# Kernel optimization log

Measured on AMD Instinct MI355X. Metric: run time of the kernel, lower is better.

The kernel has to match this reference:

```python
import jax, jax.numpy as jnp
import numpy as np

D_MODEL = 256; D_FLOW = 128; D_FFN = 1024
N_HEADS = 8; N_LEVELS = 3; N_POINTS = 4
D_HEAD = D_MODEL // N_HEADS
SHAPES = np.array([[128, 128], [64, 64], [32, 32]], dtype=np.int64)


def setup_inputs():
    key = jax.random.key(0)
    ks = jax.random.split(key, 12)
    N = 2
    LeNin = int((SHAPES[:, 0] * SHAPES[:, 1]).sum())
    Lq = int(SHAPES[0, 0] * SHAPES[0, 1])
    lsi = np.concatenate([[0], np.cumsum(SHAPES[:, 0] * SHAPES[:, 1])[:-1]])
    s = 0.02
    return {
        'src': jax.random.normal(ks[0], (N, LeNin, D_MODEL), jnp.float32),
        'flow': jax.random.normal(ks[1], (N, Lq, D_FLOW), jnp.float32),
        'spatial_shapes': jnp.asarray(SHAPES, jnp.int32),
        'level_start_index': jnp.asarray(lsi, jnp.int32),
        'w_value': jax.random.normal(ks[2], (D_MODEL, D_MODEL), jnp.float32) * s,
        'b_value': jnp.zeros((D_MODEL,), jnp.float32),
        'w_off': jax.random.normal(ks[3], (D_FLOW, N_HEADS * N_LEVELS * N_POINTS * 2), jnp.float32) * s,
        'b_off': jax.random.normal(ks[4], (N_HEADS * N_LEVELS * N_POINTS * 2,), jnp.float32) * 0.5,
        'w_attn': jax.random.normal(ks[5], (D_FLOW, N_HEADS * N_LEVELS * N_POINTS), jnp.float32) * s,
        'b_attn': jnp.zeros((N_HEADS * N_LEVELS * N_POINTS,), jnp.float32),
        'w_out': jax.random.normal(ks[6], (D_MODEL, D_MODEL), jnp.float32) * s,
        'b_out': jnp.zeros((D_MODEL,), jnp.float32),
        'gamma': jnp.ones((D_MODEL,), jnp.float32),
        'beta': jnp.zeros((D_MODEL,), jnp.float32),
        'w1': jax.random.normal(ks[7], (D_MODEL, D_FFN), jnp.float32) * s,
        'b1': jnp.zeros((D_FFN,), jnp.float32),
        'w2': jax.random.normal(ks[8], (D_FFN, D_MODEL), jnp.float32) * s,
        'b2': jnp.zeros((D_MODEL,), jnp.float32),
    }


def _bilinear_level(v, xy, H, W):
    # v: [N, nh, H*W, dh]; xy: [N, Lq, nh, np, 2] normalized to [0,1]
    # grid_sample(align_corners=False) semantics: pixel = loc * size - 0.5, zero padding
    N, Lq = xy.shape[0], xy.shape[1]
    x = xy[..., 0] * W - 0.5
    y = xy[..., 1] * H - 0.5
    x0 = jnp.floor(x); y0 = jnp.floor(y)
    dx = x - x0; dy = y - y0
    acc = jnp.zeros((N, N_HEADS, Lq * N_POINTS, v.shape[-1]), v.dtype)
    corners = ((x0, y0, (1 - dx) * (1 - dy)),
               (x0 + 1, y0, dx * (1 - dy)),
               (x0, y0 + 1, (1 - dx) * dy),
               (x0 + 1, y0 + 1, dx * dy))
    for ix, iy, w in corners:
        valid = (ix >= 0) & (ix <= W - 1) & (iy >= 0) & (iy <= H - 1)
        xi = jnp.clip(ix, 0, W - 1).astype(jnp.int32)
        yi = jnp.clip(iy, 0, H - 1).astype(jnp.int32)
        idx = (yi * W + xi).transpose(0, 2, 1, 3).reshape(N, N_HEADS, Lq * N_POINTS)
        g = jnp.take_along_axis(v, idx[..., None], axis=2)  # [N, nh, Lq*np, dh]
        wv = (w * valid).transpose(0, 2, 1, 3).reshape(N, N_HEADS, Lq * N_POINTS, 1)
        acc = acc + wv * g
    return acc


def reference(src, flow, spatial_shapes, level_start_index, w_value, b_value,
              w_off, b_off, w_attn, b_attn, w_out, b_out, gamma, beta, w1, b1, w2, b2):
    ss = np.asarray(jax.device_get(spatial_shapes))
    lsi = np.asarray(jax.device_get(level_start_index))
    N, LeNin, _ = src.shape
    Lq = flow.shape[1]
    value = (src @ w_value + b_value).reshape(N, LeNin, N_HEADS, D_HEAD)
    off = (flow @ w_off + b_off).reshape(N, Lq, N_HEADS, N_LEVELS, N_POINTS, 2)
    attn = jax.nn.softmax((flow @ w_attn + b_attn).reshape(N, Lq, N_HEADS, N_LEVELS * N_POINTS), axis=-1)
    attn = attn.reshape(N, Lq, N_HEADS, N_LEVELS, N_POINTS)
    # reference points on level-0 grid (valid_ratios == 1)
    H0, W0 = int(ss[0, 0]), int(ss[0, 1])
    ry, rx = jnp.meshgrid(jnp.linspace(0.5, H0 - 0.5, H0) / H0,
                          jnp.linspace(0.5, W0 - 0.5, W0) / W0, indexing='ij')
    ref = jnp.stack([rx.reshape(-1), ry.reshape(-1)], -1)  # [Lq, 2] (x, y)
    norm = jnp.asarray(np.stack([ss[:, 1], ss[:, 0]], -1), jnp.float32)  # [nl, 2] = (W, H)
    loc = ref[None, :, None, None, None, :] + off / norm[None, None, None, :, None, :]
    acc = jnp.zeros((N, Lq, N_HEADS, D_HEAD), src.dtype)
    for l in range(N_LEVELS):
        H, W = int(ss[l, 0]), int(ss[l, 1])
        st = int(lsi[l])
        v = value[:, st:st + H * W].transpose(0, 2, 1, 3)  # [N, nh, HW, dh]
        s_l = _bilinear_level(v, loc[:, :, :, l], H, W).reshape(N, N_HEADS, Lq, N_POINTS, D_HEAD)
        acc = acc + jnp.einsum('bhqpd,bqhp->bqhd', s_l, attn[:, :, :, l])
    src2 = acc.reshape(N, Lq, D_MODEL) @ w_out + b_out
    x = src2  # dropout is identity at inference
    mu = x.mean(-1, keepdims=True)
    var = ((x - mu) ** 2).mean(-1, keepdims=True)
    ln = (x - mu) / jnp.sqrt(var + 1e-5) * gamma + beta
    ffn = jax.nn.relu(ln @ w1 + b1) @ w2 + b2
    return x + ffn
```

## Files before the change

kernel.cpp:

```cpp
#include <hip/hip_runtime.h>
#include <cstdint>
#include <cstddef>

#define D_MODEL  256
#define D_FLOW   128
#define D_FFN    1024
#define N_HEADS  8
#define N_LEVELS 3
#define N_POINTS 4
#define D_HEAD   32
#define LQ       16384
#define LENIN    21504
#define NB       2

typedef unsigned short ushort;
typedef __attribute__((ext_vector_type(8))) short bf16x8;
typedef __attribute__((ext_vector_type(4))) float f32x4;

__device__ __forceinline__ ushort f2b(float f) {
    uint32_t u = __float_as_uint(f);
    uint32_t r = (u + 0x7fffu + ((u >> 16) & 1u)) >> 16;
    return (ushort)r;
}

__device__ __forceinline__ void gl_lds16(const void* g, void* l) {
    __builtin_amdgcn_global_load_lds(
        (const __attribute__((address_space(1))) unsigned int*)g,
        (__attribute__((address_space(3))) unsigned int*)l,
        16, 0, 0);
}

template<bool A_FP32, bool RELU, bool RESID, bool OUT_BF16>
__global__ __launch_bounds__(256)
void mfma_gemm(const void* __restrict__ Ain, const ushort* __restrict__ Bt,
               const float* __restrict__ bias, const float* __restrict__ resid,
               void* __restrict__ Cout, int N, int K)
{
    __shared__ ushort As[128 * 64];
    __shared__ ushort Bs[128 * 64];

    const int tid  = threadIdx.x;
    const int wave = tid >> 6;
    const int lane = tid & 63;
    const int quad = lane >> 4;
    const int l16  = lane & 15;
    const int wr   = (wave >> 1) * 64;
    const int wc   = (wave & 1) * 64;

    const int nx = gridDim.x;
    int lin = blockIdx.y * nx + blockIdx.x;
    const int total = nx * gridDim.y;
    if ((total & 7) == 0) lin = (lin & 7) * (total >> 3) + (lin >> 3);
    const int by = lin / nx;
    const int bx = lin - by * nx;
    const int bm = by * 128;
    const int bn = bx * 128;

    const int sr  = lane >> 3;
    const int sc  = lane & 7;
    const int gch = sc ^ sr;

    f32x4 acc[4][4] = {};
    const int swz = l16 & 7;

    for (int k0 = 0; k0 < K; k0 += 64) {
        __syncthreads();
        if (A_FP32) {
            const float* Af = (const float*)Ain;
#pragma unroll
            for (int i = 0; i < 4; ++i) {
                const int row = wave * 32 + i * 8 + sr;
                const float* p = Af + (size_t)(bm + row) * K + k0 + gch * 8;
                const float4 v0 = *(const float4*)(p);
                const float4 v1 = *(const float4*)(p + 4);
                bf16x8 pk;
                pk[0] = (short)f2b(v0.x); pk[1] = (short)f2b(v0.y);
                pk[2] = (short)f2b(v0.z); pk[3] = (short)f2b(v0.w);
                pk[4] = (short)f2b(v1.x); pk[5] = (short)f2b(v1.y);
                pk[6] = (short)f2b(v1.z); pk[7] = (short)f2b(v1.w);
                *(bf16x8*)&As[(size_t)row * 64 + sc * 8] = pk;
            }
        } else {
            const ushort* Ab = (const ushort*)Ain;
#pragma unroll
            for (int i = 0; i < 4; ++i) {
                const int row = wave * 32 + i * 8;
                gl_lds16(Ab + (size_t)(bm + row + sr) * K + k0 + gch * 8,
                         As + (size_t)row * 64);
            }
        }
#pragma unroll
        for (int i = 0; i < 4; ++i) {
            const int row = wave * 32 + i * 8;
            gl_lds16(Bt + (size_t)(bn + row + sr) * K + k0 + gch * 8,
                     Bs + (size_t)row * 64);
        }
        __syncthreads();

#pragma unroll
        for (int kk = 0; kk < 2; ++kk) {
            bf16x8 af[4], bfr[4];
#pragma unroll
            for (int mi = 0; mi < 4; ++mi) {
                const int p = (kk * 4 + quad) ^ swz;
                af[mi] = *(const bf16x8*)&As[(wr + mi * 16 + l16) * 64 + p * 8];
            }
#pragma unroll
            for (int ni = 0; ni < 4; ++ni) {
                const int p = (kk * 4 + quad) ^ swz;
                bfr[ni] = *(const bf16x8*)&Bs[(wc + ni * 16 + l16) * 64 + p * 8];
            }
#pragma unroll
            for (int mi = 0; mi < 4; ++mi)
#pragma unroll
                for (int ni = 0; ni < 4; ++ni)
                    acc[mi][ni] = __builtin_amdgcn_mfma_f32_16x16x32_bf16(
                        af[mi], bfr[ni], acc[mi][ni], 0, 0, 0);
        }
    }

#pragma unroll
    for (int mi = 0; mi < 4; ++mi) {
#pragma unroll
        for (int ni = 0; ni < 4; ++ni) {
            const int col = bn + wc + ni * 16 + l16;
            const float bb = bias[col];
#pragma unroll
            for (int r = 0; r < 4; ++r) {
                const int row = bm + wr + mi * 16 + quad * 4 + r;
                const size_t idx = (size_t)row * N + col;
                float c = acc[mi][ni][r] + bb;
                if (RELU)  c = fmaxf(c, 0.f);
                if (RESID) c += resid[idx];
                if (OUT_BF16) ((ushort*)Cout)[idx] = f2b(c);
                else          ((float*)Cout)[idx]  = c;
            }
        }
    }
}

__global__ __launch_bounds__(512, 2)
void ffn_fused_k(const ushort* __restrict__ accb, const ushort* __restrict__ woT,
                 const ushort* __restrict__ w1T,  const ushort* __restrict__ w2R,
                 const float* __restrict__ b_out, const float* __restrict__ gamma,
                 const float* __restrict__ beta,  const float* __restrict__ b1v,
                 const float* __restrict__ b2v,   float* __restrict__ out)
{
    extern __shared__ ushort smem[];
    ushort* const aS  = smem;
    ushort* const wS  = smem + 8192;
    float*  const sP  = (float*)smem;
    float*  const sQ  = (float*)(smem + 4352);
    ushort* const lnS = smem + 16384;
    float*  const sMu = (float*)(smem + 49152);
    float*  const sRi = (float*)(smem + 49408);
    ushort* const w1s0 = smem;
    ushort* const w1s1 = smem + 16384;
    ushort* const hs0  = smem + 32768;
    ushort* const hs1  = smem + 40960;

    const int tid  = threadIdx.x;
    const int wave = tid >> 6;
    const int lane = tid & 63;
    const int quad = lane >> 4;
    const int l16  = lane & 15;
    const int bm   = blockIdx.x * 128;

    const int M0   = (wave & 1) * 64;
    const int N0   = (wave >> 1) * 64;
    const int R0g1 = (wave >> 1) * 32;
    const int C0g1 = (wave & 1) * 32;

    const int sr  = lane >> 3;
    const int sc  = lane & 7;
    const int gch = sc ^ sr;

    f32x4 acc2[4][4] = {};

    for (int k0 = 0; k0 < 256; k0 += 64) {
        __syncthreads();
#pragma unroll
        for (int i = 0; i < 2; ++i) {
            const int r0 = wave * 16 + i * 8;
            gl_lds16(accb + (size_t)(bm + r0 + sr) * 256 + k0 + gch * 8,
                     aS + r0 * 64);
        }
#pragma unroll
        for (int i = 0; i < 4; ++i) {
            const int r0 = wave * 32 + i * 8;
            gl_lds16(woT + (size_t)(r0 + sr) * 256 + k0 + gch * 8,
                     wS + r0 * 64);
        }
        __syncthreads();

#pragma unroll
        for (int kk = 0; kk < 2; ++kk) {
            const int g = kk * 4 + quad;
            bf16x8 af[4], wf[4];
#pragma unroll
            for (int mt = 0; mt < 4; ++mt) {
                const int m = M0 + mt * 16 + l16;
                af[mt] = *(const bf16x8*)&aS[m * 64 + ((g ^ (m & 7)) << 3)];
            }
#pragma unroll
            for (int nt = 0; nt < 4; ++nt) {
                const int n = N0 + nt * 16 + l16;
                wf[nt] = *(const bf16x8*)&wS[n * 64 + ((g ^ (n & 7)) << 3)];
            }
#pragma unroll
            for (int mt = 0; mt < 4; ++mt)
#pragma unroll
                for (int nt = 0; nt < 4; ++nt)
                    acc2[mt][nt] = __builtin_amdgcn_mfma_f32_16x16x32_bf16(
                        wf[nt], af[mt], acc2[mt][nt], 0, 0, 0);
        }
    }
    __syncthreads();

    {
        float4 bo[4];
#pragma unroll
        for (int nt = 0; nt < 4; ++nt)
            bo[nt] = *(const float4*)&b_out[N0 + nt * 16 + quad * 4];
        const int widx = (wave >> 1) * 4 + quad;
#pragma unroll
        for (int mt = 0; mt < 4; ++mt) {
            const int m = M0 + mt * 16 + l16;
            float s = 0.f, s2 = 0.f;
#pragma unroll
            for (int nt = 0; nt < 4; ++nt) {
                acc2[mt][nt][0] += bo[nt].x;
                acc2[mt][nt][1] += bo[nt].y;
                acc2[mt][nt][2] += bo[nt].z;
                acc2[mt][nt][3] += bo[nt].w;
#pragma unroll
                for (int r = 0; r < 4; ++r) {
                    const float c = acc2[mt][nt][r];
                    s += c; s2 += c * c;
                }
            }
            sP[m * 17 + widx] = s;
            sQ[m * 17 + widx] = s2;
        }
    }
    __syncthreads();

    if (tid < 128) {
        float s = 0.f, s2 = 0.f;
#pragma unroll
        for (int j = 0; j < 16; ++j) { s += sP[tid * 17 + j]; s2 += sQ[tid * 17 + j]; }
        const float mu  = s * (1.f / 256.f);
        const float var = s2 * (1.f / 256.f) - mu * mu;
        sMu[tid] = mu;
        sRi[tid] = rsqrtf(var + 1e-5f);
    }
    __syncthreads();

    float mu4[4], ri4[4];
#pragma unroll
    for (int mt = 0; mt < 4; ++mt) {
        const int m = M0 + mt * 16 + l16;
        mu4[mt] = sMu[m]; ri4[mt] = sRi[m];
    }

#pragma unroll
    for (int i = 0; i < 4; ++i) {
        const int r0 = (wave * 4 + i) * 2;
        const int r  = r0 + (lane >> 5);
        gl_lds16(w1T + (size_t)r * 256 + (((lane & 31) ^ (r & 7)) << 3),
                 w1s0 + r0 * 256);
    }

#pragma unroll
    for (int mt = 0; mt < 4; ++mt) {
        const int m = M0 + mt * 16 + l16;
        const float mu = mu4[mt], ri = ri4[mt];
#pragma unroll
        for (int nt = 0; nt < 4; ++nt) {
            const int col0 = N0 + nt * 16 + quad * 4;
            const float4 g4 = *(const float4*)&gamma[col0];
            const float4 b4 = *(const float4*)&beta[col0];
            ushort4 pk;
            pk.x = f2b((acc2[mt][nt][0] - mu) * ri * g4.x + b4.x);
            pk.y = f2b((acc2[mt][nt][1] - mu) * ri * g4.y + b4.y);
            pk.z = f2b((acc2[mt][nt][2] - mu) * ri * g4.z + b4.z);
            pk.w = f2b((acc2[mt][nt][3] - mu) * ri * g4.w + b4.w);
            const int c8 = col0 >> 3;
            *(ushort4*)&lnS[m * 256 + ((c8 ^ (m & 7)) << 3) + (quad & 1) * 4] = pk;
        }
    }
    __syncthreads();

    bf16x8 afA[2][8];
#pragma unroll
    for (int mt = 0; mt < 2; ++mt)
#pragma unroll
        for (int kk = 0; kk < 8; ++kk) {
            const int row = R0g1 + mt * 16 + l16;
            afA[mt][kk] = *(const bf16x8*)
                &lnS[row * 256 + (((kk * 4 + quad) ^ (row & 7)) << 3)];
        }
    __syncthreads();

#pragma unroll 1
    for (int c = 0; c < 16; ++c) {
        ushort* const w1cur = (c & 1) ? w1s1 : w1s0;
        ushort* const w1nxt = (c & 1) ? w1s0 : w1s1;
        ushort* const hcur  = (c & 1) ? hs1  : hs0;
        ushort* const hprv  = (c & 1) ? hs0  : hs1;

        if (c < 15) {
#pragma unroll
            for (int i = 0; i < 4; ++i) {
                const int r0 = (wave * 4 + i) * 2;
                const int r  = r0 + (lane >> 5);
                gl_lds16(w1T + (size_t)((c + 1) * 64 + r) * 256
                             + (((lane & 31) ^ (r & 7)) << 3),
                         w1nxt + r0 * 256);
            }
        }

        bf16x8 w2f[2][4];
        if (c >= 1) {
#pragma unroll
            for (int kk = 0; kk < 2; ++kk) {
                const int g = kk * 4 + quad;
                const ushort* base = w2R + ((size_t)((c - 1) * 8 + g)) * 2048;
#pragma unroll
                for (int nt = 0; nt < 4; ++nt) {
                    const int n = N0 + nt * 16 + l16;
                    w2f[kk][nt] = *(const bf16x8*)(base + n * 8);
                }
            }
        }

        f32x4 acc1[2][2] = {};
#pragma unroll
        for (int kk = 0; kk < 8; ++kk) {
            bf16x8 wf[2];
#pragma unroll
            for (int nt = 0; nt < 2; ++nt) {
                const int n = C0g1 + nt * 16 + l16;
                wf[nt] = *(const bf16x8*)
                    &w1cur[n * 256 + (((kk * 4 + quad) ^ (n & 7)) << 3)];
            }
#pragma unroll
            for (int mt = 0; mt < 2; ++mt)
#pragma unroll
                for (int nt = 0; nt < 2; ++nt)
                    acc1[mt][nt] = __builtin_amdgcn_mfma_f32_16x16x32_bf16(
                        wf[nt], afA[mt][kk], acc1[mt][nt], 0, 0, 0);
        }

        {
            float4 bb[2];
#pragma unroll
            for (int nt = 0; nt < 2; ++nt)
                bb[nt] = *(const float4*)&b1v[c * 64 + C0g1 + nt * 16 + quad * 4];
#pragma unroll
            for (int mt = 0; mt < 2; ++mt) {
                const int m = R0g1 + mt * 16 + l16;
#pragma unroll
                for (int nt = 0; nt < 2; ++nt) {
                    const int oct = (C0g1 >> 2) + nt * 4 + quad;
                    ushort4 pk;
                    pk.x = f2b(fmaxf(acc1[mt][nt][0] + bb[nt].x, 0.f));
                    pk.y = f2b(fmaxf(acc1[mt][nt][1] + bb[nt].y, 0.f));
                    pk.z = f2b(fmaxf(acc1[mt][nt][2] + bb[nt].z, 0.f));
                    pk.w = f2b(fmaxf(acc1[mt][nt][3] + bb[nt].w, 0.f));
                    *(ushort4*)&hcur[m * 64 + ((oct ^ ((m & 7) << 1)) << 2)] = pk;
                }
            }
        }

        if (c >= 1) {
#pragma unroll
            for (int kk = 0; kk < 2; ++kk) {
                const int g = kk * 4 + quad;
                bf16x8 hf[4];
#pragma unroll
                for (int mt = 0; mt < 4; ++mt) {
                    const int m = M0 + mt * 16 + l16;
                    hf[mt] = *(const bf16x8*)&hprv[m * 64 + ((g ^ (m & 7)) << 3)];
                }
#pragma unroll
                for (int mt = 0; mt < 4; ++mt)
#pragma unroll
                    for (int nt = 0; nt < 4; ++nt)
                        acc2[mt][nt] = __builtin_amdgcn_mfma_f32_16x16x32_bf16(
                            w2f[kk][nt], hf[mt], acc2[mt][nt], 0, 0, 0);
            }
        }
        __syncthreads();
    }

    {
        bf16x8 w2f[2][4];
#pragma unroll
        for (int kk = 0; kk < 2; ++kk) {
            const int g = kk * 4 + quad;
            const ushort* base = w2R + ((size_t)(15 * 8 + g)) * 2048;
#pragma unroll
            for (int nt = 0; nt < 4; ++nt) {
                const int n = N0 + nt * 16 + l16;
                w2f[kk][nt] = *(const bf16x8*)(base + n * 8);
            }
        }
#pragma unroll
        for (int kk = 0; kk < 2; ++kk) {
            const int g = kk * 4 + quad;
            bf16x8 hf[4];
#pragma unroll
            for (int mt = 0; mt < 4; ++mt) {
                const int m = M0 + mt * 16 + l16;
                hf[mt] = *(const bf16x8*)&hs1[m * 64 + ((g ^ (m & 7)) << 3)];
            }
#pragma unroll
            for (int mt = 0; mt < 4; ++mt)
#pragma unroll
                for (int nt = 0; nt < 4; ++nt)
                    acc2[mt][nt] = __builtin_amdgcn_mfma_f32_16x16x32_bf16(
                        w2f[kk][nt], hf[mt], acc2[mt][nt], 0, 0, 0);
        }
    }

#pragma unroll
    for (int mt = 0; mt < 4; ++mt) {
        const int row = bm + M0 + mt * 16 + l16;
#pragma unroll
        for (int nt = 0; nt < 4; ++nt) {
            const int col = N0 + nt * 16 + quad * 4;
            const float4 b4 = *(const float4*)&b2v[col];
            float4 v;
            v.x = acc2[mt][nt][0] + b4.x;
            v.y = acc2[mt][nt][1] + b4.y;
            v.z = acc2[mt][nt][2] + b4.z;
            v.w = acc2[mt][nt][3] + b4.w;
            *(float4*)(out + (size_t)row * 256 + col) = v;
        }
    }
}

__device__ __forceinline__ void acc8(float* a, uint4 g, float w) {
    a[0] = fmaf(w, __uint_as_float(g.x << 16), a[0]);
    a[1] = fmaf(w, __uint_as_float(g.x), a[1]);
    a[2] = fmaf(w, __uint_as_float(g.y << 16), a[2]);
    a[3] = fmaf(w, __uint_as_float(g.y), a[3]);
    a[4] = fmaf(w, __uint_as_float(g.z << 16), a[4]);
    a[5] = fmaf(w, __uint_as_float(g.z), a[5]);
    a[6] = fmaf(w, __uint_as_float(g.w << 16), a[6]);
    a[7] = fmaf(w, __uint_as_float(g.w), a[7]);
}

__global__ __launch_bounds__(256)
void sample_k(const ushort* __restrict__ value, const ushort* __restrict__ projc,
              ushort* __restrict__ acc)
{
    __shared__ float sOff[8][192];
    __shared__ float sAttn[8][96];

    const int tid = threadIdx.x;
    const int bid = blockIdx.x;
    const int bq0 = (((bid & 7) << 9) | (bid >> 3)) << 3;

    for (int i = tid; i < 8 * 288; i += 256) {
        const int qw = i / 288, j = i - qw * 288;
        const float v = __uint_as_float((uint32_t)projc[(size_t)(bq0 + qw) * 384 + j] << 16);
        if (j < 192) sOff[qw][j] = v;
        else         sAttn[qw][j - 192] = v;
    }
    __syncthreads();

    if (tid < 64) {
        const int qw = tid >> 3, h = tid & 7;
        float* row = &sAttn[qw][h * 12];
        float m = row[0];
#pragma unroll
        for (int j = 1; j < 12; ++j) m = fmaxf(m, row[j]);
        float s = 0.f;
#pragma unroll
        for (int j = 0; j < 12; ++j) { const float e = __expf(row[j] - m); row[j] = e; s += e; }
        const float inv = 1.f / s;
#pragma unroll
        for (int j = 0; j < 12; ++j) row[j] *= inv;
    }
    __syncthreads();

    const int wave = tid >> 6, lane = tid & 63;
    const int qh = lane >> 5;
    const int h  = (lane >> 2) & 7;
    const int cg = lane & 3;
    const int qw = wave * 2 + qh;
    const int bq = bq0 + qw;
    const int n  = bq >> 14;
    const int q  = bq & 16383;

    const float qx = (float)(q & 127) + 0.5f;
    const float qy = (float)(q >> 7) + 0.5f;

    const int LSIc[3] = {0, 16384, 20480};

    float a[8] = {0.f, 0.f, 0.f, 0.f, 0.f, 0.f, 0.f, 0.f};
    const ushort* vbase = value + (size_t)n * LENIN * D_MODEL + h * D_HEAD + cg * 8;

#pragma unroll
    for (int l = 0; l < N_LEVELS; ++l) {
        const int   W     = 128 >> l;
        const int   SH    = 7 - l;
        const float scale = 1.f / (float)(1 << l);
        const float cx    = qx * scale - 0.5f;
        const float cy    = qy * scale - 0.5f;
        const ushort* vlev = vbase + ((size_t)LSIc[l] << 8);
#pragma unroll
        for (int p = 0; p < N_POINTS; ++p) {
            const int ob = (h * N_LEVELS + l) * (N_POINTS * 2) + p * 2;
            const float aw = sAttn[qw][h * 12 + l * 4 + p];
            const float x = cx + sOff[qw][ob];
            const float y = cy + sOff[qw][ob + 1];
            const float x0f = floorf(x), y0f = floorf(y);
            const int x0 = (int)x0f, y0 = (int)y0f;
            const float dx = x - x0f, dy = y - y0f;
            float wx1 = dx * aw, wx0 = aw - wx1;
            float wy1 = dy,      wy0 = 1.f - dy;
            if ((unsigned)x0       > (unsigned)(W - 1)) wx0 = 0.f;
            if ((unsigned)(x0 + 1) > (unsigned)(W - 1)) wx1 = 0.f;
            if ((unsigned)y0       > (unsigned)(W - 1)) wy0 = 0.f;
            if ((unsigned)(y0 + 1) > (unsigned)(W - 1)) wy1 = 0.f;
            const int xi0 = min(max(x0, 0), W - 1);
            const int xi1 = min(max(x0 + 1, 0), W - 1);
            const int yi0 = min(max(y0, 0), W - 1);
            const int yi1 = min(max(y0 + 1, 0), W - 1);
            const uint4 g00 = *(const uint4*)(vlev + ((size_t)((yi0 << SH) + xi0) << 8));
            const uint4 g01 = *(const uint4*)(vlev + ((size_t)((yi0 << SH) + xi1) << 8));
            const uint4 g10 = *(const uint4*)(vlev + ((size_t)((yi1 << SH) + xi0) << 8));
            const uint4 g11 = *(const uint4*)(vlev + ((size_t)((yi1 << SH) + xi1) << 8));
            acc8(a, g00, wx0 * wy0);
            acc8(a, g01, wx1 * wy0);
            acc8(a, g10, wx0 * wy1);
            acc8(a, g11, wx1 * wy1);
        }
    }

    const uint32_t o0 = (uint32_t)f2b(a[0]) | ((uint32_t)f2b(a[1]) << 16);
    const uint32_t o1 = (uint32_t)f2b(a[2]) | ((uint32_t)f2b(a[3]) << 16);
    const uint32_t o2 = (uint32_t)f2b(a[4]) | ((uint32_t)f2b(a[5]) << 16);
    const uint32_t o3 = (uint32_t)f2b(a[6]) | ((uint32_t)f2b(a[7]) << 16);
    const uint4 ov = {o0, o1, o2, o3};
    *(uint4*)(acc + (size_t)bq * D_MODEL + h * D_HEAD + cg * 8) = ov;
}

__global__ __launch_bounds__(256)
void prep_all_k(const float* __restrict__ w_value, const float* __restrict__ w_out,
                const float* __restrict__ w1, const float* __restrict__ w2,
                const float* __restrict__ w_off, const float* __restrict__ b_off,
                const float* __restrict__ w_attn, const float* __restrict__ b_attn,
                ushort* __restrict__ wvT, ushort* __restrict__ woT,
                ushort* __restrict__ w1T, ushort* __restrict__ w2R,
                ushort* __restrict__ wcT, float* __restrict__ biasc)
{
    int i = blockIdx.x * 256 + threadIdx.x;
    if (i < 65536) {
        const int k = i >> 8, n = i & 255;
        wvT[(size_t)n * 256 + k] = f2b(w_value[i]);
        return;
    }
    i -= 65536;
    if (i < 65536) {
        const int k = i >> 8, n = i & 255;
        woT[(size_t)n * 256 + k] = f2b(w_out[i]);
        return;
    }
    i -= 65536;
    if (i < 262144) {
        const int k = i >> 10, n = i & 1023;
        w1T[(size_t)n * 256 + k] = f2b(w1[i]);
        return;
    }
    i -= 262144;
    if (i < 262144) {
        const int k = i >> 8, n = i & 255;
        w2R[(size_t)(k >> 3) * 2048 + n * 8 + (k & 7)] = f2b(w2[i]);
        return;
    }
    i -= 262144;
    if (i < 49152) {
        const int nn = i >> 7, k = i & 127;
        float v = 0.f;
        if (nn < 192)      v = w_off[(size_t)k * 192 + nn];
        else if (nn < 288) v = w_attn[(size_t)k * 96 + (nn - 192)];
        wcT[i] = f2b(v);
        return;
    }
    i -= 49152;
    if (i < 384) {
        float b = 0.f;
        if (i < 192)      b = b_off[i];
        else if (i < 288) b = b_attn[i - 192];
        biasc[i] = b;
    }
}

extern "C" void kernel_launch(void* const* d_in, const int* in_sizes, int n_in,
                              void* d_out, int out_size, void* d_ws, size_t ws_size,
                              hipStream_t stream)
{
    const float* src     = (const float*)d_in[0];
    const float* flow    = (const float*)d_in[1];
    const float* w_value = (const float*)d_in[4];
    const float* b_value = (const float*)d_in[5];
    const float* w_off   = (const float*)d_in[6];
    const float* b_off   = (const float*)d_in[7];
    const float* w_attn  = (const float*)d_in[8];
    const float* b_attn  = (const float*)d_in[9];
    const float* w_out   = (const float*)d_in[10];
    const float* b_out   = (const float*)d_in[11];
    const float* gamma   = (const float*)d_in[12];
    const float* beta    = (const float*)d_in[13];
    const float* w1      = (const float*)d_in[14];
    const float* b1      = (const float*)d_in[15];
    const float* w2      = (const float*)d_in[16];
    const float* b2      = (const float*)d_in[17];
    float* out = (float*)d_out;
    char*  wsb = (char*)d_ws;

    ushort* value_bf = (ushort*)(wsb);
    ushort* acc_bf   = (ushort*)(wsb + 22020096);
    ushort* projc_bf = (ushort*)(wsb + 67108864);
    ushort* wvT      = (ushort*)(wsb + 92274688);
    ushort* woT      = (ushort*)(wsb + 92405760);
    ushort* w1T      = (ushort*)(wsb + 92536832);
    ushort* w2R      = (ushort*)(wsb + 93061120);
    ushort* wcT      = (ushort*)(wsb + 93585408);
    float*  biasc    = (float*) (wsb + 93683712);

    const int Mq = NB * LQ;
    const int Mv = NB * LENIN;

    static bool ffn_attr_done = false;
    if (!ffn_attr_done) {
        hipFuncSetAttribute((const void*)ffn_fused_k,
                            hipFuncAttributeMaxDynamicSharedMemorySize, 99328);
        ffn_attr_done = true;
    }

    prep_all_k<<<2754, 256, 0, stream>>>(w_value, w_out, w1, w2,
                                         w_off, b_off, w_attn, b_attn,
                                         wvT, woT, w1T, w2R, wcT, biasc);

    mfma_gemm<true, false, false, true><<<dim3(2, Mv / 128), 256, 0, stream>>>(
        src, wvT, b_value, nullptr, value_bf, 256, 256);

    mfma_gemm<true, false, false, true><<<dim3(3, Mq / 128), 256, 0, stream>>>(
        flow, wcT, biasc, nullptr, projc_bf, 384, 128);

    sample_k<<<Mq / 8, 256, 0, stream>>>(value_bf, projc_bf, acc_bf);

    ffn_fused_k<<<Mq / 128, 512, 99328, stream>>>(
        acc_bf, woT, w1T, w2R, b_out, gamma, beta, b1, b2, out);
}
```

Measured before the change: 250.4 us.

## Load FFN W1 fragments directly from global in MFMA layout instead of LDS

```diff
diff --git a/kernel.cpp b/kernel.cpp
--- a/kernel.cpp
+++ b/kernel.cpp
@@ -141,7 +141,7 @@
 
 __global__ __launch_bounds__(512, 2)
 void ffn_fused_k(const ushort* __restrict__ accb, const ushort* __restrict__ woT,
-                 const ushort* __restrict__ w1T,  const ushort* __restrict__ w2R,
+                 const ushort* __restrict__ w1F,  const ushort* __restrict__ w2R,
                  const float* __restrict__ b_out, const float* __restrict__ gamma,
                  const float* __restrict__ beta,  const float* __restrict__ b1v,
                  const float* __restrict__ b2v,   float* __restrict__ out)
@@ -154,10 +154,8 @@
     ushort* const lnS = smem + 16384;
     float*  const sMu = (float*)(smem + 49152);
     float*  const sRi = (float*)(smem + 49408);
-    ushort* const w1s0 = smem;
-    ushort* const w1s1 = smem + 16384;
-    ushort* const hs0  = smem + 32768;
-    ushort* const hs1  = smem + 40960;
+    ushort* const hs0 = smem;
+    ushort* const hs1 = smem + 8192;
 
     const int tid  = threadIdx.x;
     const int wave = tid >> 6;
@@ -261,14 +259,6 @@
     for (int mt = 0; mt < 4; ++mt) {
         const int m = M0 + mt * 16 + l16;
         mu4[mt] = sMu[m]; ri4[mt] = sRi[m];
-    }
-
-#pragma unroll
-    for (int i = 0; i < 4; ++i) {
-        const int r0 = (wave * 4 + i) * 2;
-        const int r  = r0 + (lane >> 5);
-        gl_lds16(w1T + (size_t)r * 256 + (((lane & 31) ^ (r & 7)) << 3),
-                 w1s0 + r0 * 256);
     }
 
 #pragma unroll
@@ -302,23 +292,13 @@
         }
     __syncthreads();
 
+    const int n1a = C0g1 + l16;
+    const int n1b = C0g1 + 16 + l16;
+
 #pragma unroll 1
     for (int c = 0; c < 16; ++c) {
-        ushort* const w1cur = (c & 1) ? w1s1 : w1s0;
-        ushort* const w1nxt = (c & 1) ? w1s0 : w1s1;
-        ushort* const hcur  = (c & 1) ? hs1  : hs0;
-        ushort* const hprv  = (c & 1) ? hs0  : hs1;
-
-        if (c < 15) {
-#pragma unroll
-            for (int i = 0; i < 4; ++i) {
-                const int r0 = (wave * 4 + i) * 2;
-                const int r  = r0 + (lane >> 5);
-                gl_lds16(w1T + (size_t)((c + 1) * 64 + r) * 256
-                             + (((lane & 31) ^ (r & 7)) << 3),
-                         w1nxt + r0 * 256);
-            }
-        }
+        ushort* const hcur = (c & 1) ? hs1 : hs0;
+        ushort* const hprv = (c & 1) ? hs0 : hs1;
 
         bf16x8 w2f[2][4];
         if (c >= 1) {
@@ -334,22 +314,48 @@
             }
         }
 
+        bf16x8 w1p[2][2];
+        {
+            const ushort* base = w1F + ((size_t)quad << 13) + (size_t)c * 64 * 8;
+            w1p[0][0] = *(const bf16x8*)(base + n1a * 8);
+            w1p[0][1] = *(const bf16x8*)(base + n1b * 8);
+        }
+
+        if (c >= 1) {
+#pragma unroll
+            for (int kk = 0; kk < 2; ++kk) {
+                const int g = kk * 4 + quad;
+                bf16x8 hf[4];
+#pragma unroll
+                for (int mt = 0; mt < 4; ++mt) {
+                    const int m = M0 + mt * 16 + l16;
+                    hf[mt] = *(const bf16x8*)&hprv[m * 64 + ((g ^ (m & 7)) << 3)];
+                }
+#pragma unroll
+                for (int mt = 0; mt < 4; ++mt)
+#pragma unroll
+                    for (int nt = 0; nt < 4; ++nt)
+                        acc2[mt][nt] = __builtin_amdgcn_mfma_f32_16x16x32_bf16(
+                            w2f[kk][nt], hf[mt], acc2[mt][nt], 0, 0, 0);
+            }
+        }
+
         f32x4 acc1[2][2] = {};
 #pragma unroll
         for (int kk = 0; kk < 8; ++kk) {
-            bf16x8 wf[2];
-#pragma unroll
-            for (int nt = 0; nt < 2; ++nt) {
-                const int n = C0g1 + nt * 16 + l16;
-                wf[nt] = *(const bf16x8*)
-                    &w1cur[n * 256 + (((kk * 4 + quad) ^ (n & 7)) << 3)];
+            const int cur = kk & 1, nxt = cur ^ 1;
+            if (kk < 7) {
+                const int g = (kk + 1) * 4 + quad;
+                const ushort* base = w1F + ((size_t)g << 13) + (size_t)c * 64 * 8;
+                w1p[nxt][0] = *(const bf16x8*)(base + n1a * 8);
+                w1p[nxt][1] = *(const bf16x8*)(base + n1b * 8);
             }
 #pragma unroll
             for (int mt = 0; mt < 2; ++mt)
 #pragma unroll
                 for (int nt = 0; nt < 2; ++nt)
                     acc1[mt][nt] = __builtin_amdgcn_mfma_f32_16x16x32_bf16(
-                        wf[nt], afA[mt][kk], acc1[mt][nt], 0, 0, 0);
+                        w1p[cur][nt], afA[mt][kk], acc1[mt][nt], 0, 0, 0);
         }
 
         {
@@ -370,25 +376,6 @@
                     pk.w = f2b(fmaxf(acc1[mt][nt][3] + bb[nt].w, 0.f));
                     *(ushort4*)&hcur[m * 64 + ((oct ^ ((m & 7) << 1)) << 2)] = pk;
                 }
-            }
-        }
-
-        if (c >= 1) {
-#pragma unroll
-            for (int kk = 0; kk < 2; ++kk) {
-                const int g = kk * 4 + quad;
-                bf16x8 hf[4];
-#pragma unroll
-                for (int mt = 0; mt < 4; ++mt) {
-                    const int m = M0 + mt * 16 + l16;
-                    hf[mt] = *(const bf16x8*)&hprv[m * 64 + ((g ^ (m & 7)) << 3)];
-                }
-#pragma unroll
-                for (int mt = 0; mt < 4; ++mt)
-#pragma unroll
-                    for (int nt = 0; nt < 4; ++nt)
-                        acc2[mt][nt] = __builtin_amdgcn_mfma_f32_16x16x32_bf16(
-                            w2f[kk][nt], hf[mt], acc2[mt][nt], 0, 0, 0);
             }
         }
         __syncthreads();
@@ -555,7 +542,7 @@
                 const float* __restrict__ w_off, const float* __restrict__ b_off,
                 const float* __restrict__ w_attn, const float* __restrict__ b_attn,
                 ushort* __restrict__ wvT, ushort* __restrict__ woT,
-                ushort* __restrict__ w1T, ushort* __restrict__ w2R,
+                ushort* __restrict__ w1F, ushort* __restrict__ w2R,
                 ushort* __restrict__ wcT, float* __restrict__ biasc)
 {
     int i = blockIdx.x * 256 + threadIdx.x;
@@ -573,7 +560,7 @@
     i -= 65536;
     if (i < 262144) {
         const int k = i >> 10, n = i & 1023;
-        w1T[(size_t)n * 256 + k] = f2b(w1[i]);
+        w1F[(size_t)(k >> 3) * 8192 + n * 8 + (k & 7)] = f2b(w1[i]);
         return;
     }
     i -= 262144;
@@ -628,7 +615,7 @@
     ushort* projc_bf = (ushort*)(wsb + 67108864);
     ushort* wvT      = (ushort*)(wsb + 92274688);
     ushort* woT      = (ushort*)(wsb + 92405760);
-    ushort* w1T      = (ushort*)(wsb + 92536832);
+    ushort* w1F      = (ushort*)(wsb + 92536832);
     ushort* w2R      = (ushort*)(wsb + 93061120);
     ushort* wcT      = (ushort*)(wsb + 93585408);
     float*  biasc    = (float*) (wsb + 93683712);
@@ -645,7 +632,7 @@
 
     prep_all_k<<<2754, 256, 0, stream>>>(w_value, w_out, w1, w2,
                                          w_off, b_off, w_attn, b_attn,
-                                         wvT, woT, w1T, w2R, wcT, biasc);
+                                         wvT, woT, w1F, w2R, wcT, biasc);
 
     mfma_gemm<true, false, false, true><<<dim3(2, Mv / 128), 256, 0, stream>>>(
         src, wvT, b_value, nullptr, value_bf, 256, 256);
@@ -656,5 +643,5 @@
     sample_k<<<Mq / 8, 256, 0, stream>>>(value_bf, projc_bf, acc_bf);
 
     ffn_fused_k<<<Mq / 128, 512, 99328, stream>>>(
-        acc_bf, woT, w1T, w2R, b_out, gamma, beta, b1, b2, out);
-}
+        acc_bf, woT, w1F, w2R, b_out, gamma, beta, b1, b2, out);
+}
```

Measured after the change: 254.9 us. Within noise of the previous version (+1.8%).
